# Performance work log

Measured on AMD Instinct MI355X. Metric: run time of the kernel, lower is better.

The kernel has to match this reference:

```python
import jax, jax.numpy as jnp
import numpy as np

B, C, N, D = 8, 32, 128, 1024


def setup_inputs() -> dict:
    key = jax.random.key(0)
    x = jax.random.normal(key, (B, C, N, D), dtype=jnp.float32)
    return {"x": x}


def _gram_schmidt(x):
    # x: [B, C, N, D]. Sequentially orthogonalize vector i against vectors 0..i-1.
    n = x.shape[2]
    row_idx = jnp.arange(n)  # [N]

    def step(x, i):
        xi = jax.lax.dynamic_slice_in_dim(x, i, 1, axis=2)          # [B,C,1,D]
        dots = jnp.sum(xi * x, axis=3, keepdims=True)                # [B,C,N,1]
        nrm2 = jnp.sum(x * x, axis=3, keepdims=True)                 # [B,C,N,1]
        proj = dots / nrm2 * x                                       # [B,C,N,D]
        # only project onto the already-processed vectors 0..i-1
        mask = (row_idx < i)[None, None, :, None]
        corr = jnp.sum(jnp.where(mask, proj, 0.0), axis=2, keepdims=True)  # [B,C,1,D]
        # original torch code subtracts a .detach()-ed correction
        corr = jax.lax.stop_gradient(corr)
        x = jax.lax.dynamic_update_slice_in_dim(x, xi - corr, i, axis=2)
        return x, None

    x, _ = jax.lax.scan(step, x, jnp.arange(1, n))
    # note: torch normalizes by the norm over dim=2 (across the N vectors)
    return x / jnp.linalg.norm(x, axis=2, keepdims=True)


def reference(x):
    return _gram_schmidt(x)
```

## Files before the change

kernel.cpp:

```cpp
#include <hip/hip_runtime.h>
#include <math.h>

#define D 1024
#define NROW 128
#define PANEL 16
#define NPANELS 8
#define NTHREADS 1024
#define GP 132
#define XSP 136
#define WPITCH 17
#define RPITCH 132

#define R1_OFF 67584
#define R2_OFF 135168
#define SMEM_BYTES (R2_OFF + 18944)

typedef __attribute__((ext_vector_type(8))) short short8;
typedef __attribute__((ext_vector_type(4))) float floatx4;

__device__ __forceinline__ unsigned short f2bf(float f) {
  unsigned int u = __builtin_bit_cast(unsigned int, f);
  u += 0x7fffu + ((u >> 16) & 1u);
  return (unsigned short)(u >> 16);
}

__global__ __launch_bounds__(NTHREADS, 4) void gs_kernel(const float* __restrict__ xg_all,
                                                         float* __restrict__ qg_all) {
  __shared__ __align__(16) char smem[SMEM_BYTES];
  float (*G)[GP] = (float(*)[GP])(smem);
  unsigned short (*XT)[XSP] = (unsigned short(*)[XSP])(smem);
  float (*T)[GP] = (float(*)[GP])(smem + R1_OFF);
  unsigned short (*Xs)[XSP] = (unsigned short(*)[XSP])(smem + R1_OFF);
  unsigned short (*Tb)[XSP] = (unsigned short(*)[XSP])(smem + R1_OFF);
  float (*W)[WPITCH] = (float(*)[WPITCH])(smem + R2_OFF);
  float (*R)[RPITCH] = (float(*)[RPITCH])(smem + R2_OFF + 7616);
  float* Scr = (float*)(smem + R2_OFF);
  float (*Gm)[16] = (float(*)[16])(smem + R2_OFF + 16384);
  float (*LT)[16] = (float(*)[16])(smem + R2_OFF + 17408);
  float* rinv = (float*)(smem + R2_OFF + 18432);

  const int t = threadIdx.x;
  const int lane = t & 63;
  const int w = t >> 6;
  const int m = lane & 15;
  const int kb = lane >> 4;
  const size_t off = (size_t)blockIdx.x * (NROW * D);
  const float* xg = xg_all + off;
  float* qg = qg_all + off;

  int ti0, tj0, ti1, tj1, ti2 = 0, tj2 = 0;
  {
    int id = w, ti = 0;
    while ((ti + 1) * (ti + 2) / 2 <= id) ++ti;
    ti0 = ti; tj0 = id - ti * (ti + 1) / 2;
    id = w + 16; ti = 0;
    while ((ti + 1) * (ti + 2) / 2 <= id) ++ti;
    ti1 = ti; tj1 = id - ti * (ti + 1) / 2;
    if (w < 4) {
      id = w + 32; ti = 0;
      while ((ti + 1) * (ti + 2) / 2 <= id) ++ti;
      ti2 = ti; tj2 = id - ti * (ti + 1) / 2;
    }
  }
  floatx4 ga0 = {0.f, 0.f, 0.f, 0.f}, ga1 = {0.f, 0.f, 0.f, 0.f}, ga2 = {0.f, 0.f, 0.f, 0.f};

#define GFRAG(TI, TJ, ACC) do { \
    _Pragma("unroll") \
    for (int s4 = 0; s4 < 4; ++s4) { \
      const int kk = s4 * 32 + kb * 8; \
      const short8 a_ = *(const short8*)&Xs[(TI) * 16 + m][kk]; \
      const short8 b_ = *(const short8*)&Xs[(TJ) * 16 + m][kk]; \
      ACC = __builtin_amdgcn_mfma_f32_16x16x32_bf16(a_, b_, ACC, 0, 0, 0); \
    } } while (0)

  for (int ks = 0; ks < 8; ++ks) {
#pragma unroll
    for (int qi = 0; qi < 4; ++qi) {
      const int idx = qi * 1024 + t;
      const int row = idx >> 5;
      const int c4 = (idx & 31) << 2;
      const float4 v = *(const float4*)(xg + (size_t)row * D + ks * 128 + c4);
      ushort4 u;
      u.x = f2bf(v.x); u.y = f2bf(v.y); u.z = f2bf(v.z); u.w = f2bf(v.w);
      *(ushort4*)&Xs[row][c4] = u;
    }
    __syncthreads();
    GFRAG(ti0, tj0, ga0);
    GFRAG(ti1, tj1, ga1);
    if (w < 4) GFRAG(ti2, tj2, ga2);
    __syncthreads();
  }
#define GWRITE(TI, TJ, ACC) do { \
    _Pragma("unroll") \
    for (int r = 0; r < 4; ++r) { \
      const int gr = (TI) * 16 + kb * 4 + r, gc = (TJ) * 16 + m; \
      G[gr][gc] = ACC[r]; \
      if ((TI) != (TJ)) G[gc][gr] = ACC[r]; \
    } } while (0)
  GWRITE(ti0, tj0, ga0);
  GWRITE(ti1, tj1, ga1);
  if (w < 4) GWRITE(ti2, tj2, ga2);
  __syncthreads();

  for (int k = 0; k < NPANELS; ++k) {
    const int i0 = k * PANEL;

    if (k > 0) {
#pragma unroll
      for (int jb = 0; jb < 2; ++jb) {
        const int j = jb * 64 + (t >> 4);
        if (j < i0) {
          const int p = t & 15;
          float s = 0.f;
          for (int mm = 0; mm <= j; ++mm)
            s += T[j][mm] * G[mm][i0 + p];
          W[j][p] = s;
        }
      }
    }
    __syncthreads();

    {
      const int col = t & 127;
      const int m8 = t >> 7;
      const int jst = (w & 1) << 6;
#pragma unroll
      for (int h = 0; h < 2; ++h) {
        const int mm = m8 + 8 * h;
        float r = (col == i0 + mm) ? 1.0f : 0.0f;
        for (int j = jst; j < i0; ++j)
          r -= (W[j][mm] * rinv[j]) * T[j][col];
        R[mm][col] = r;
      }
    }
    if (t < 256) {
      const int p = t >> 4, q = t & 15;
      float s = G[i0 + p][i0 + q];
      for (int j = 0; j < i0; ++j)
        s -= rinv[j] * W[j][p] * W[j][q];
      Gm[p][q] = s;
    }
    __syncthreads();

    if (t < 64) {
      const int r = t & 15;
      float Lreg[PANEL];
      float rn[PANEL];
#pragma unroll
      for (int mq = 0; mq < PANEL; ++mq) {
        const float g = Gm[r][mq];
        float accL = (r == mq) ? 1.0f : 0.0f;
        float nm = Gm[mq][mq];
#pragma unroll
        for (int j = 0; j < mq; ++j) {
          float p = Lreg[j] * g;
          p += __shfl_xor(p, 1);
          p += __shfl_xor(p, 2);
          p += __shfl_xor(p, 4);
          p += __shfl_xor(p, 8);
          const float cj = p * rn[j];
          accL -= cj * Lreg[j];
          nm -= cj * p;
        }
        Lreg[mq] = accL;
        rn[mq] = 1.0f / nm;
        if (t == 0) rinv[i0 + mq] = rn[mq];
      }
      if (t < 16) {
#pragma unroll
        for (int mq = 0; mq < PANEL; ++mq) LT[r][mq] = Lreg[mq];
      }
    }
    __syncthreads();

    {
      const int col = t & 127;
      const int i8 = t >> 7;
#pragma unroll
      for (int h = 0; h < 2; ++h) {
        const int ii = i8 + 8 * h;
        float s = 0.f;
#pragma unroll
        for (int mm = 0; mm < PANEL; ++mm)
          s += LT[mm][ii] * R[mm][col];
        T[i0 + ii][col] = s;
      }
    }
    __syncthreads();
  }

  {
    float tvv[16];
#pragma unroll
    for (int i = 0; i < 16; ++i) {
      const int idx = (i << 10) + t;
      tvv[i] = T[idx >> 7][idx & 127];
    }
    __syncthreads();
#pragma unroll
    for (int i = 0; i < 16; ++i) {
      const int idx = (i << 10) + t;
      Tb[idx >> 7][idx & 127] = f2bf(tvv[i]);
    }
  }

  const int tro = w >> 1;
  const int tch = (w & 1) << 2;

#define TXSQ(S, QA) \
    Scr[((tch + (S)) * 16 + m) * 33 + tro * 4 + kb] = \
        QA[0] * QA[0] + QA[1] * QA[1] + QA[2] * QA[2] + QA[3] * QA[3];
#define TXST(S, QA) do { \
    const int gc_ = cb * 128 + (tch + (S)) * 16 + m; \
    const float iv_ = rinv[(tch + (S)) * 16 + m]; \
    _Pragma("unroll") \
    for (int r = 0; r < 4; ++r) \
      qg[(size_t)(tro * 16 + kb * 4 + r) * D + gc_] = QA[r] * iv_; \
  } while (0)

  for (int cb = 0; cb < 8; ++cb) {
    __syncthreads();
#pragma unroll
    for (int i = 0; i < 4; ++i) {
      const int r = i * 32 + (t >> 5);
      const int c4 = (t & 31) << 2;
      const float4 v = *(const float4*)(xg + (size_t)r * D + cb * 128 + c4);
      XT[c4 + 0][r] = f2bf(v.x);
      XT[c4 + 1][r] = f2bf(v.y);
      XT[c4 + 2][r] = f2bf(v.z);
      XT[c4 + 3][r] = f2bf(v.w);
    }
    __syncthreads();
    floatx4 qa0 = {0.f, 0.f, 0.f, 0.f}, qa1 = {0.f, 0.f, 0.f, 0.f};
    floatx4 qa2 = {0.f, 0.f, 0.f, 0.f}, qa3 = {0.f, 0.f, 0.f, 0.f};
#pragma unroll
    for (int s4 = 0; s4 < 4; ++s4) {
      const int kk = s4 * 32 + kb * 8;
      const short8 a = *(const short8*)&Tb[tro * 16 + m][kk];
      const short8 b0 = *(const short8*)&XT[(tch + 0) * 16 + m][kk];
      const short8 b1 = *(const short8*)&XT[(tch + 1) * 16 + m][kk];
      const short8 b2 = *(const short8*)&XT[(tch + 2) * 16 + m][kk];
      const short8 b3 = *(const short8*)&XT[(tch + 3) * 16 + m][kk];
      qa0 = __builtin_amdgcn_mfma_f32_16x16x32_bf16(a, b0, qa0, 0, 0, 0);
      qa1 = __builtin_amdgcn_mfma_f32_16x16x32_bf16(a, b1, qa1, 0, 0, 0);
      qa2 = __builtin_amdgcn_mfma_f32_16x16x32_bf16(a, b2, qa2, 0, 0, 0);
      qa3 = __builtin_amdgcn_mfma_f32_16x16x32_bf16(a, b3, qa3, 0, 0, 0);
    }
    TXSQ(0, qa0); TXSQ(1, qa1); TXSQ(2, qa2); TXSQ(3, qa3);
    __syncthreads();
    if (t < 128) {
      float ssum = 0.f;
#pragma unroll
      for (int i = 0; i < 32; ++i) ssum += Scr[t * 33 + i];
      rinv[t] = 1.0f / sqrtf(ssum);
    }
    __syncthreads();
    TXST(0, qa0); TXST(1, qa1); TXST(2, qa2); TXST(3, qa3);
  }
}

extern "C" void kernel_launch(void* const* d_in, const int* in_sizes, int n_in,
                              void* d_out, int out_size, void* d_ws, size_t ws_size,
                              hipStream_t stream) {
  const float* x = (const float*)d_in[0];
  float* out = (float*)d_out;
  gs_kernel<<<dim3(256), dim3(NTHREADS), 0, stream>>>(x, out);
}
```

Baseline: 410.8 us.

## Double-buffer X slices with register prefetch, swizzle XT, transpose W panel

The Gram and output phases now prefetch the next slice of x into registers while the current slice is converted to bf16 into one of two alternating LDS buffers. This removes one barrier per iteration and overlaps global loads with MFMA work. The transposed X tile is written with a 4x4 register transpose and an XOR swizzle to reduce bank conflicts, where before it used scalar scattered stores. The W panel is stored transposed (WT) and computed with vectorized float4 reads, and the R and Gm loops are unrolled. Shared memory is re-laid out with separate regions, and the larger footprint may lower occupancy.

```diff
diff --git a/kernel.cpp b/kernel.cpp
--- a/kernel.cpp
+++ b/kernel.cpp
@@ -6,14 +6,19 @@
 #define PANEL 16
 #define NPANELS 8
 #define NTHREADS 1024
-#define GP 132
+#define GPITCH 132
 #define XSP 136
-#define WPITCH 17
-#define RPITCH 132
-
-#define R1_OFF 67584
-#define R2_OFF 135168
-#define SMEM_BYTES (R2_OFF + 18944)
+
+#define T_OFF    67584
+#define WT_OFF   135168
+#define R_OFF    143616
+#define GM_OFF   152064
+#define LT_OFF   153088
+#define RINV_OFF 154112
+#define SMEM_BYTES 154624
+#define XBUF_SZ  34816
+#define TB_OFF   69632
+#define SCR_OFF  104448
 
 typedef __attribute__((ext_vector_type(8))) short short8;
 typedef __attribute__((ext_vector_type(4))) float floatx4;
@@ -27,17 +32,15 @@
 __global__ __launch_bounds__(NTHREADS, 4) void gs_kernel(const float* __restrict__ xg_all,
                                                          float* __restrict__ qg_all) {
   __shared__ __align__(16) char smem[SMEM_BYTES];
-  float (*G)[GP] = (float(*)[GP])(smem);
-  unsigned short (*XT)[XSP] = (unsigned short(*)[XSP])(smem);
-  float (*T)[GP] = (float(*)[GP])(smem + R1_OFF);
-  unsigned short (*Xs)[XSP] = (unsigned short(*)[XSP])(smem + R1_OFF);
-  unsigned short (*Tb)[XSP] = (unsigned short(*)[XSP])(smem + R1_OFF);
-  float (*W)[WPITCH] = (float(*)[WPITCH])(smem + R2_OFF);
-  float (*R)[RPITCH] = (float(*)[RPITCH])(smem + R2_OFF + 7616);
-  float* Scr = (float*)(smem + R2_OFF);
-  float (*Gm)[16] = (float(*)[16])(smem + R2_OFF + 16384);
-  float (*LT)[16] = (float(*)[16])(smem + R2_OFF + 17408);
-  float* rinv = (float*)(smem + R2_OFF + 18432);
+  float (*G)[GPITCH] = (float(*)[GPITCH])(smem);
+  float (*T)[GPITCH] = (float(*)[GPITCH])(smem + T_OFF);
+  float (*WT)[GPITCH] = (float(*)[GPITCH])(smem + WT_OFF);
+  float (*R)[GPITCH] = (float(*)[GPITCH])(smem + R_OFF);
+  float (*Gm)[16] = (float(*)[16])(smem + GM_OFF);
+  float (*LT)[16] = (float(*)[16])(smem + LT_OFF);
+  float* rinv = (float*)(smem + RINV_OFF);
+  unsigned short (*Tb)[XSP] = (unsigned short(*)[XSP])(smem + TB_OFF);
+  float* Scr = (float*)(smem + SCR_OFF);
 
   const int t = threadIdx.x;
   const int lane = t & 63;
@@ -63,35 +66,45 @@
     }
   }
   floatx4 ga0 = {0.f, 0.f, 0.f, 0.f}, ga1 = {0.f, 0.f, 0.f, 0.f}, ga2 = {0.f, 0.f, 0.f, 0.f};
-
-#define GFRAG(TI, TJ, ACC) do { \
-    _Pragma("unroll") \
+  float4 xr[4];
+
+#define LDSLICE(KS) do { _Pragma("unroll") \
+    for (int qi = 0; qi < 4; ++qi) { \
+      const int idx = qi * 1024 + t; \
+      const int row = idx >> 5; \
+      const int c4 = (idx & 31) << 2; \
+      xr[qi] = *(const float4*)(xg + (size_t)row * D + (KS) * 128 + c4); \
+    } } while (0)
+#define XCOMMIT(BB) do { _Pragma("unroll") \
+    for (int qi = 0; qi < 4; ++qi) { \
+      const int idx = qi * 1024 + t; \
+      const int row = idx >> 5; \
+      const int c4 = (idx & 31) << 2; \
+      ushort4 u_; \
+      u_.x = f2bf(xr[qi].x); u_.y = f2bf(xr[qi].y); \
+      u_.z = f2bf(xr[qi].z); u_.w = f2bf(xr[qi].w); \
+      *(ushort4*)((BB) + row * 272 + c4 * 2) = u_; \
+    } } while (0)
+#define GFRAG(BB, TI, TJ, ACC) do { _Pragma("unroll") \
     for (int s4 = 0; s4 < 4; ++s4) { \
       const int kk = s4 * 32 + kb * 8; \
-      const short8 a_ = *(const short8*)&Xs[(TI) * 16 + m][kk]; \
-      const short8 b_ = *(const short8*)&Xs[(TJ) * 16 + m][kk]; \
+      const short8 a_ = *(const short8*)((BB) + ((TI) * 16 + m) * 272 + kk * 2); \
+      const short8 b_ = *(const short8*)((BB) + ((TJ) * 16 + m) * 272 + kk * 2); \
       ACC = __builtin_amdgcn_mfma_f32_16x16x32_bf16(a_, b_, ACC, 0, 0, 0); \
     } } while (0)
 
+  LDSLICE(0);
   for (int ks = 0; ks < 8; ++ks) {
-#pragma unroll
-    for (int qi = 0; qi < 4; ++qi) {
-      const int idx = qi * 1024 + t;
-      const int row = idx >> 5;
-      const int c4 = (idx & 31) << 2;
-      const float4 v = *(const float4*)(xg + (size_t)row * D + ks * 128 + c4);
-      ushort4 u;
-      u.x = f2bf(v.x); u.y = f2bf(v.y); u.z = f2bf(v.z); u.w = f2bf(v.w);
-      *(ushort4*)&Xs[row][c4] = u;
-    }
-    __syncthreads();
-    GFRAG(ti0, tj0, ga0);
-    GFRAG(ti1, tj1, ga1);
-    if (w < 4) GFRAG(ti2, tj2, ga2);
-    __syncthreads();
-  }
-#define GWRITE(TI, TJ, ACC) do { \
-    _Pragma("unroll") \
+    char* sb = smem + (ks & 1) * XBUF_SZ;
+    XCOMMIT(sb);
+    if (ks < 7) LDSLICE(ks + 1);
+    __syncthreads();
+    GFRAG(sb, ti0, tj0, ga0);
+    GFRAG(sb, ti1, tj1, ga1);
+    if (w < 4) GFRAG(sb, ti2, tj2, ga2);
+  }
+  __syncthreads();
+#define GWRITE(TI, TJ, ACC) do { _Pragma("unroll") \
     for (int r = 0; r < 4; ++r) { \
       const int gr = (TI) * 16 + kb * 4 + r, gc = (TJ) * 16 + m; \
       G[gr][gc] = ACC[r]; \
@@ -106,38 +119,53 @@
     const int i0 = k * PANEL;
 
     if (k > 0) {
-#pragma unroll
-      for (int jb = 0; jb < 2; ++jb) {
-        const int j = jb * 64 + (t >> 4);
-        if (j < i0) {
-          const int p = t & 15;
-          float s = 0.f;
-          for (int mm = 0; mm <= j; ++mm)
-            s += T[j][mm] * G[mm][i0 + p];
-          W[j][p] = s;
-        }
-      }
+      const int jA = t & 63, j2 = jA + 64;
+      float s1 = 0.f, s2 = 0.f;
+      for (int mb = 0; mb < i0; mb += 8) {
+        const float4 g0 = *(const float4*)&G[i0 + w][mb];
+        const float4 g1 = *(const float4*)&G[i0 + w][mb + 4];
+        const float4 a0 = *(const float4*)&T[jA][mb];
+        const float4 a1 = *(const float4*)&T[jA][mb + 4];
+        const float4 b0 = *(const float4*)&T[j2][mb];
+        const float4 b1 = *(const float4*)&T[j2][mb + 4];
+        s1 += a0.x * g0.x; s1 += a0.y * g0.y; s1 += a0.z * g0.z; s1 += a0.w * g0.w;
+        s1 += a1.x * g1.x; s1 += a1.y * g1.y; s1 += a1.z * g1.z; s1 += a1.w * g1.w;
+        s2 += b0.x * g0.x; s2 += b0.y * g0.y; s2 += b0.z * g0.z; s2 += b0.w * g0.w;
+        s2 += b1.x * g1.x; s2 += b1.y * g1.y; s2 += b1.z * g1.z; s2 += b1.w * g1.w;
+      }
+      if (jA < i0) WT[w][jA] = s1;
+      if (j2 < i0) WT[w][j2] = s2;
     }
     __syncthreads();
 
     {
       const int col = t & 127;
-      const int m8 = t >> 7;
-      const int jst = (w & 1) << 6;
-#pragma unroll
-      for (int h = 0; h < 2; ++h) {
-        const int mm = m8 + 8 * h;
-        float r = (col == i0 + mm) ? 1.0f : 0.0f;
-        for (int j = jst; j < i0; ++j)
-          r -= (W[j][mm] * rinv[j]) * T[j][col];
-        R[mm][col] = r;
-      }
-    }
-    if (t < 256) {
-      const int p = t >> 4, q = t & 15;
+      const int mh = t >> 7, mh8 = mh + 8;
+      float s0 = (col == i0 + mh) ? 1.0f : 0.0f;
+      float s1 = (col == i0 + mh8) ? 1.0f : 0.0f;
+      for (int jb = 0; jb < i0; jb += 8) {
+#pragma unroll
+        for (int u = 0; u < 8; ++u) {
+          const int j = jb + u;
+          const float tv = T[j][col];
+          const float rv = rinv[j];
+          s0 -= (WT[mh][j] * rv) * tv;
+          s1 -= (WT[mh8][j] * rv) * tv;
+        }
+      }
+      R[mh][col] = s0;
+      R[mh8][col] = s1;
+    }
+    if (t >= 768) {
+      const int p = (t >> 4) & 15, q = t & 15;
       float s = G[i0 + p][i0 + q];
-      for (int j = 0; j < i0; ++j)
-        s -= rinv[j] * W[j][p] * W[j][q];
+      for (int jb = 0; jb < i0; jb += 8) {
+#pragma unroll
+        for (int u = 0; u < 8; ++u) {
+          const int j = jb + u;
+          s -= rinv[j] * WT[p][j] * WT[q][j];
+        }
+      }
       Gm[p][q] = s;
     }
     __syncthreads();
@@ -204,8 +232,18 @@
     }
   }
 
+  const int qq = t & 31;
+  const int r0 = (t >> 5) << 2;
   const int tro = w >> 1;
   const int tch = (w & 1) << 2;
+  float4 xt0, xt1, xt2, xt3;
+  {
+    const float* s = xg + (size_t)r0 * D + qq * 4;
+    xt0 = *(const float4*)(s);
+    xt1 = *(const float4*)(s + D);
+    xt2 = *(const float4*)(s + 2 * D);
+    xt3 = *(const float4*)(s + 3 * D);
+  }
 
 #define TXSQ(S, QA) \
     Scr[((tch + (S)) * 16 + m) * 33 + tro * 4 + kb] = \
@@ -219,16 +257,26 @@
   } while (0)
 
   for (int cb = 0; cb < 8; ++cb) {
-    __syncthreads();
-#pragma unroll
-    for (int i = 0; i < 4; ++i) {
-      const int r = i * 32 + (t >> 5);
-      const int c4 = (t & 31) << 2;
-      const float4 v = *(const float4*)(xg + (size_t)r * D + cb * 128 + c4);
-      XT[c4 + 0][r] = f2bf(v.x);
-      XT[c4 + 1][r] = f2bf(v.y);
-      XT[c4 + 2][r] = f2bf(v.z);
-      XT[c4 + 3][r] = f2bf(v.w);
+    char* xb = smem + (cb & 1) * XBUF_SZ;
+    {
+      const int sw = (qq & 7) << 4;
+      ushort4 c0, c1, c2, c3;
+      c0.x = f2bf(xt0.x); c0.y = f2bf(xt1.x); c0.z = f2bf(xt2.x); c0.w = f2bf(xt3.x);
+      c1.x = f2bf(xt0.y); c1.y = f2bf(xt1.y); c1.z = f2bf(xt2.y); c1.w = f2bf(xt3.y);
+      c2.x = f2bf(xt0.z); c2.y = f2bf(xt1.z); c2.z = f2bf(xt2.z); c2.w = f2bf(xt3.z);
+      c3.x = f2bf(xt0.w); c3.y = f2bf(xt1.w); c3.z = f2bf(xt2.w); c3.w = f2bf(xt3.w);
+      const int cb0 = qq * 4;
+      *(ushort4*)(xb + (((cb0 + 0) * 272 + r0 * 2) ^ sw)) = c0;
+      *(ushort4*)(xb + (((cb0 + 1) * 272 + r0 * 2) ^ sw)) = c1;
+      *(ushort4*)(xb + (((cb0 + 2) * 272 + r0 * 2) ^ sw)) = c2;
+      *(ushort4*)(xb + (((cb0 + 3) * 272 + r0 * 2) ^ sw)) = c3;
+    }
+    if (cb < 7) {
+      const float* s = xg + (size_t)r0 * D + (cb + 1) * 128 + qq * 4;
+      xt0 = *(const float4*)(s);
+      xt1 = *(const float4*)(s + D);
+      xt2 = *(const float4*)(s + 2 * D);
+      xt3 = *(const float4*)(s + 3 * D);
     }
     __syncthreads();
     floatx4 qa0 = {0.f, 0.f, 0.f, 0.f}, qa1 = {0.f, 0.f, 0.f, 0.f};
@@ -236,11 +284,13 @@
 #pragma unroll
     for (int s4 = 0; s4 < 4; ++s4) {
       const int kk = s4 * 32 + kb * 8;
-      const short8 a = *(const short8*)&Tb[tro * 16 + m][kk];
-      const short8 b0 = *(const short8*)&XT[(tch + 0) * 16 + m][kk];
-      const short8 b1 = *(const short8*)&XT[(tch + 1) * 16 + m][kk];
-      const short8 b2 = *(const short8*)&XT[(tch + 2) * 16 + m][kk];
-      const short8 b3 = *(const short8*)&XT[(tch + 3) * 16 + m][kk];
+      const short8 a = *(const short8*)((char*)Tb + (tro * 16 + m) * 272 + kk * 2);
+      const int c0_ = (tch + 0) * 16 + m, c1_ = (tch + 1) * 16 + m;
+      const int c2_ = (tch + 2) * 16 + m, c3_ = (tch + 3) * 16 + m;
+      const short8 b0 = *(const short8*)(xb + ((c0_ * 272 + kk * 2) ^ (((c0_ >> 2) & 7) << 4)));
+      const short8 b1 = *(const short8*)(xb + ((c1_ * 272 + kk * 2) ^ (((c1_ >> 2) & 7) << 4)));
+      const short8 b2 = *(const short8*)(xb + ((c2_ * 272 + kk * 2) ^ (((c2_ >> 2) & 7) << 4)));
+      const short8 b3 = *(const short8*)(xb + ((c3_ * 272 + kk * 2) ^ (((c3_ >> 2) & 7) << 4)));
       qa0 = __builtin_amdgcn_mfma_f32_16x16x32_bf16(a, b0, qa0, 0, 0, 0);
       qa1 = __builtin_amdgcn_mfma_f32_16x16x32_bf16(a, b1, qa1, 0, 0, 0);
       qa2 = __builtin_amdgcn_mfma_f32_16x16x32_bf16(a, b2, qa2, 0, 0, 0);
```

Measured after the change: 374.7 us. 1.1x faster.
